# Kernel optimization log

Hardware: AMD Instinct MI355X
Metric: run time of the kernel (lower is better)

The kernel has to match this reference:

```python
import jax, jax.numpy as jnp
import numpy as np

INPUT_SIZE = 128
HIDDEN_SIZE = 128
BATCH = 65536


def _xavier(key, shape):
    fan_out, fan_in = shape
    limit = np.sqrt(6.0 / (fan_in + fan_out)).astype(np.float32)
    return jax.random.uniform(key, shape, jnp.float32, -limit, limit)


def setup_inputs() -> dict:
    key = jax.random.key(0)
    ks = jax.random.split(key, 12)
    inp = {
        "x": jax.random.normal(ks[0], (BATCH, INPUT_SIZE), jnp.float32),
        "h_t": jax.random.normal(ks[1], (BATCH, HIDDEN_SIZE), jnp.float32),
        "c_t": jax.random.normal(ks[2], (BATCH, HIDDEN_SIZE), jnp.float32),
        "W_ii": _xavier(ks[3], (HIDDEN_SIZE, INPUT_SIZE)),
        "W_hi": _xavier(ks[4], (HIDDEN_SIZE, HIDDEN_SIZE)),
        "b_i": jnp.zeros((HIDDEN_SIZE,), jnp.float32),
        "W_if": _xavier(ks[5], (HIDDEN_SIZE, INPUT_SIZE)),
        "W_hf": _xavier(ks[6], (HIDDEN_SIZE, HIDDEN_SIZE)),
        "b_f": jnp.zeros((HIDDEN_SIZE,), jnp.float32),
        "W_ig": _xavier(ks[7], (HIDDEN_SIZE, INPUT_SIZE)),
        "W_hg": _xavier(ks[8], (HIDDEN_SIZE, HIDDEN_SIZE)),
        "b_g": jnp.zeros((HIDDEN_SIZE,), jnp.float32),
        "W_io": _xavier(ks[9], (HIDDEN_SIZE, INPUT_SIZE)),
        "W_ho": _xavier(ks[10], (HIDDEN_SIZE, HIDDEN_SIZE)),
        "b_o": jnp.zeros((HIDDEN_SIZE,), jnp.float32),
    }
    return inp


def reference(x, h_t, c_t, W_ii, W_hi, b_i, W_if, W_hf, b_f, W_ig, W_hg, b_g, W_io, W_ho, b_o):
    # Fuse the 8 small GEMMs into 2 concatenated GEMMs, identical math to
    # per-gate F.linear calls (same weights, just stacked along output dim).
    W_x = jnp.concatenate([W_ii, W_if, W_ig, W_io], axis=0)   # [4H, I]
    W_h = jnp.concatenate([W_hi, W_hf, W_hg, W_ho], axis=0)   # [4H, H]
    b = jnp.concatenate([b_i, b_f, b_g, b_o], axis=0)         # [4H]
    gates = x @ W_x.T + h_t @ W_h.T + b                       # [B, 4H]
    i_a, f_a, g_a, o_a = jnp.split(gates, 4, axis=1)
    i_t = jax.nn.sigmoid(i_a)
    f_t = jax.nn.sigmoid(f_a)
    g_t = jnp.tanh(g_a)
    o_t = jax.nn.sigmoid(o_a)
    c_new = f_t * c_t + i_t * g_t
    h_new = o_t * jnp.tanh(c_new)
    return (h_new, c_new)
```

## Files before the change

### kernel.cpp

```cpp
#include <hip/hip_runtime.h>
#include <hip/hip_bf16.h>


typedef short s16x8 __attribute__((ext_vector_type(8)));
typedef float f32x4 __attribute__((ext_vector_type(4)));

__device__ __forceinline__ short f2bf(float f) {
    __hip_bfloat16 h = __float2bfloat16(f);
    return __builtin_bit_cast(short, h);
}
__device__ __forceinline__ float sigm(float x) { return 1.0f / (1.0f + __expf(-x)); }
__device__ __forceinline__ float tanh_f(float x) { return 1.0f - 2.0f / (1.0f + __expf(2.0f * x)); }

__device__ __forceinline__ void dma16(const float* g, void* lds) {
    __builtin_amdgcn_global_load_lds(
        (const __attribute__((address_space(1))) void*)g,
        (__attribute__((address_space(3))) void*)lds, 16, 0, 0);
}

__global__ __launch_bounds__(256)
void repack_weights(const float* __restrict__ Wii, const float* __restrict__ Whi,
                    const float* __restrict__ Wif, const float* __restrict__ Whf,
                    const float* __restrict__ Wig, const float* __restrict__ Whg,
                    const float* __restrict__ Wio, const float* __restrict__ Who,
                    short* __restrict__ ws)
{
    const int t   = blockIdx.x * 256 + threadIdx.x;
    const int fi  = t >> 6;
    const int l   = t & 63;
    const int ks  = fi & 7;
    const int g   = (fi >> 3) & 3;
    const int jt  = fi >> 5;
    const int j   = jt * 16 + (l & 15);
    const int k   = ks * 32 + (l >> 4) * 8;

    const float* wx = (g == 0) ? Wii : (g == 1) ? Wif : (g == 2) ? Wig : Wio;
    const float* wh = (g == 0) ? Whi : (g == 1) ? Whf : (g == 2) ? Whg : Who;
    const float* src = (k < 128) ? (wx + (size_t)j * 128 + k)
                                 : (wh + (size_t)j * 128 + (k - 128));
    f32x4 a = *(const f32x4*)src;
    f32x4 b = *(const f32x4*)(src + 4);
    s16x8 v;
#pragma unroll
    for (int q = 0; q < 4; ++q) { v[q] = f2bf(a[q]); v[4 + q] = f2bf(b[q]); }
    *(s16x8*)(ws + (size_t)t * 8) = v;
}

__global__ __launch_bounds__(512, 2)
void lstm_cell_kernel(const float* __restrict__ X,
                      const float* __restrict__ H,
                      const float* __restrict__ C,
                      const float* __restrict__ Bi, const float* __restrict__ Bf,
                      const float* __restrict__ Bg, const float* __restrict__ Bo,
                      const short* __restrict__ WS,
                      float* __restrict__ OutH,
                      float* __restrict__ OutC)
{
    __shared__ __align__(16) char sA[65536];

    const int tid = threadIdx.x;
    const int l   = tid & 63;
    const int w   = tid >> 6;
    const int lj  = l & 15;
    const int lq  = l >> 4;
    const int jw  = w * 16 + lj;
    const int tile0 = blockIdx.x * 8;

    s16x8 wreg[4][8];
    {
        const short* wp = WS + (size_t)(w * 4) * 8 * 512 + l * 8;
#pragma unroll
        for (int g = 0; g < 4; ++g)
#pragma unroll
            for (int ks = 0; ks < 8; ++ks)
                wreg[g][ks] = *(const s16x8*)(wp + (size_t)(g * 8 + ks) * 512);
    }
    const float bi  = Bi[jw];
    const float bfv = Bf[jw];
    const float bg  = Bg[jw];
    const float bo  = Bo[jw];

    const int   ci    = l & 31;
    const float* abase = (l >= 32) ? H : X;

    auto STAGE = [&](int t) {
        const int B0 = (tile0 + t) * 32;
        char* dst = sA + (t & 1) * 32768;
#pragma unroll
        for (int r = 0; r < 4; ++r) {
            const int m = w * 4 + r;
            const float* src = abase + (size_t)(B0 + m) * 128 + ((ci ^ (m & 7)) << 2);
            dma16(src, dst + m * 1024);
        }
    };

    float cp[2][8];
    auto CLOAD = [&](int t, float* c) {
        const int B0 = (tile0 + t) * 32;
#pragma unroll
        for (int mt = 0; mt < 2; ++mt)
#pragma unroll
            for (int r = 0; r < 4; ++r)
                c[mt * 4 + r] = C[(size_t)(B0 + mt * 16 + lq * 4 + r) * 128 + jw];
    };

    STAGE(0);  CLOAD(0, cp[0]);
    STAGE(1);  CLOAD(1, cp[1]);

#pragma unroll 2
    for (int t = 0; t < 8; ++t) {
        if (t == 0)      asm volatile("s_waitcnt vmcnt(0)" ::: "memory");
        else if (t == 7) asm volatile("s_waitcnt vmcnt(16)" ::: "memory");
        else             asm volatile("s_waitcnt vmcnt(28)" ::: "memory");
        __builtin_amdgcn_sched_barrier(0);
        __builtin_amdgcn_s_barrier();
        __builtin_amdgcn_sched_barrier(0);

        const char* sb = sA + (t & 1) * 32768;

        f32x4 acc[2][4];
#pragma unroll
        for (int mt = 0; mt < 2; ++mt)
#pragma unroll
            for (int g = 0; g < 4; ++g)
                acc[mt][g] = (f32x4){0.f, 0.f, 0.f, 0.f};

#pragma unroll
        for (int ks = 0; ks < 8; ++ks) {
            s16x8 af[2];
#pragma unroll
            for (int mt = 0; mt < 2; ++mt) {
                const int m  = mt * 16 + lj;
                const int cg = ks * 8 + lq * 2;
                const int p0 = (cg & 32) | ((cg & 31) ^ (m & 7));
                const f32x4 q0 = *(const f32x4*)(sb + m * 1024 + p0 * 16);
                const f32x4 q1 = *(const f32x4*)(sb + m * 1024 + (p0 ^ 1) * 16);
                s16x8 v;
#pragma unroll
                for (int q = 0; q < 4; ++q) { v[q] = f2bf(q0[q]); v[4 + q] = f2bf(q1[q]); }
                af[mt] = v;
            }
#pragma unroll
            for (int g = 0; g < 4; ++g) {
                acc[0][g] = __builtin_amdgcn_mfma_f32_16x16x32_bf16(af[0], wreg[g][ks], acc[0][g], 0, 0, 0);
                acc[1][g] = __builtin_amdgcn_mfma_f32_16x16x32_bf16(af[1], wreg[g][ks], acc[1][g], 0, 0, 0);
            }
        }

        __builtin_amdgcn_sched_barrier(0);
        __builtin_amdgcn_s_barrier();
        __builtin_amdgcn_sched_barrier(0);

        {
            const int B0 = (tile0 + t) * 32;
#pragma unroll
            for (int mt = 0; mt < 2; ++mt) {
#pragma unroll
                for (int r = 0; r < 4; ++r) {
                    const int b = B0 + mt * 16 + lq * 4 + r;
                    const size_t idx = (size_t)b * 128 + jw;
                    const float ia = acc[mt][0][r] + bi;
                    const float fa = acc[mt][1][r] + bfv;
                    const float ga = acc[mt][2][r] + bg;
                    const float oa = acc[mt][3][r] + bo;
                    const float it = sigm(ia);
                    const float ft = sigm(fa);
                    const float gt = tanh_f(ga);
                    const float ot = sigm(oa);
                    const float co = cp[t & 1][mt * 4 + r];
                    const float cn = ft * co + it * gt;
                    const float hn = ot * tanh_f(cn);
                    OutH[idx] = hn;
                    OutC[idx] = cn;
                }
            }
        }

        __builtin_amdgcn_sched_barrier(0);
        if (t < 6) {
            STAGE(t + 2);
            CLOAD(t + 2, cp[t & 1]);
        }
        __builtin_amdgcn_sched_barrier(0);
    }
}

extern "C" void kernel_launch(void* const* d_in, const int* in_sizes, int n_in,
                              void* d_out, int out_size, void* d_ws, size_t ws_size,
                              hipStream_t stream) {
    const float* X   = (const float*)d_in[0];
    const float* H   = (const float*)d_in[1];
    const float* C   = (const float*)d_in[2];
    const float* Wii = (const float*)d_in[3];
    const float* Whi = (const float*)d_in[4];
    const float* Bi  = (const float*)d_in[5];
    const float* Wif = (const float*)d_in[6];
    const float* Whf = (const float*)d_in[7];
    const float* Bf  = (const float*)d_in[8];
    const float* Wig = (const float*)d_in[9];
    const float* Whg = (const float*)d_in[10];
    const float* Bg  = (const float*)d_in[11];
    const float* Wio = (const float*)d_in[12];
    const float* Who = (const float*)d_in[13];
    const float* Bo  = (const float*)d_in[14];

    short* ws = (short*)d_ws;

    hipLaunchKernelGGL(repack_weights, dim3(64), dim3(256), 0, stream,
                       Wii, Whi, Wif, Whf, Wig, Whg, Wio, Who, ws);

    float* OutH = (float*)d_out;
    float* OutC = OutH + (size_t)65536 * 128;

    hipLaunchKernelGGL(lstm_cell_kernel, dim3(256), dim3(512), 0, stream,
                       X, H, C, Bi, Bf, Bg, Bo, ws, OutH, OutC);
}
```

Baseline: 185.0 us.

## Stage activations as bf16 in LDS via registers and halve per-block work

Replaces the direct global-to-LDS DMA of fp32 activations with register loads that are converted to bf16 before being written to LDS in MFMA fragment order, halving the LDS footprint and removing per-k-step conversions and swizzle math. Only half the weight fragments stay resident in registers; the other half are reloaded from global memory each tile to cut register pressure. The launch bound rises to 4 blocks per CU and the grid doubles to 512 blocks of 4 tiles each, aiming for more occupancy to hide latency. In exchange the kernel drops its explicit two-deep DMA prefetch and waitcnt scheduling, and the C load is no longer prefetched a tile ahead.

```diff
diff --git a/kernel.cpp b/kernel.cpp
--- a/kernel.cpp
+++ b/kernel.cpp
@@ -11,12 +11,6 @@
 }
 __device__ __forceinline__ float sigm(float x) { return 1.0f / (1.0f + __expf(-x)); }
 __device__ __forceinline__ float tanh_f(float x) { return 1.0f - 2.0f / (1.0f + __expf(2.0f * x)); }
-
-__device__ __forceinline__ void dma16(const float* g, void* lds) {
-    __builtin_amdgcn_global_load_lds(
-        (const __attribute__((address_space(1))) void*)g,
-        (__attribute__((address_space(3))) void*)lds, 16, 0, 0);
-}
 
 __global__ __launch_bounds__(256)
 void repack_weights(const float* __restrict__ Wii, const float* __restrict__ Whi,
@@ -46,7 +40,7 @@
     *(s16x8*)(ws + (size_t)t * 8) = v;
 }
 
-__global__ __launch_bounds__(512, 2)
+__global__ __launch_bounds__(512, 4)
 void lstm_cell_kernel(const float* __restrict__ X,
                       const float* __restrict__ H,
                       const float* __restrict__ C,
@@ -56,7 +50,7 @@
                       float* __restrict__ OutH,
                       float* __restrict__ OutC)
 {
-    __shared__ __align__(16) char sA[65536];
+    __shared__ __align__(16) char sA[32768];
 
     const int tid = threadIdx.x;
     const int l   = tid & 63;
@@ -64,59 +58,76 @@
     const int lj  = l & 15;
     const int lq  = l >> 4;
     const int jw  = w * 16 + lj;
-    const int tile0 = blockIdx.x * 8;
-
-    s16x8 wreg[4][8];
-    {
-        const short* wp = WS + (size_t)(w * 4) * 8 * 512 + l * 8;
-#pragma unroll
-        for (int g = 0; g < 4; ++g)
-#pragma unroll
-            for (int ks = 0; ks < 8; ++ks)
-                wreg[g][ks] = *(const s16x8*)(wp + (size_t)(g * 8 + ks) * 512);
-    }
+    const int tile0 = blockIdx.x * 4;
+
+    const short* wsw = WS + (size_t)(w * 4) * 8 * 512 + (size_t)l * 8;
+    s16x8 wlo[4][4];
+#pragma unroll
+    for (int g = 0; g < 4; ++g)
+#pragma unroll
+        for (int ks = 0; ks < 4; ++ks)
+            wlo[g][ks] = *(const s16x8*)(wsw + (size_t)(g * 8 + ks) * 512);
+
     const float bi  = Bi[jw];
     const float bfv = Bf[jw];
     const float bg  = Bg[jw];
     const float bo  = Bo[jw];
 
-    const int   ci    = l & 31;
-    const float* abase = (l >= 32) ? H : X;
-
-    auto STAGE = [&](int t) {
+    const float* sbase = (w < 4) ? X : H;
+    const int    colr  = (w & 3) * 32 + lq * 8;
+
+    f32x4 sa[2][2], sb[2][2];
+
+    {
+        const int B0 = tile0 * 32;
+#pragma unroll
+        for (int mt = 0; mt < 2; ++mt) {
+            const float* p = sbase + (size_t)(B0 + mt * 16 + lj) * 128 + colr;
+            sa[0][mt] = *(const f32x4*)p;
+            sb[0][mt] = *(const f32x4*)(p + 4);
+        }
+    }
+
+#pragma unroll
+    for (int t = 0; t < 4; ++t) {
+        char* buf = sA + (t & 1) * 16384;
+
+#pragma unroll
+        for (int mt = 0; mt < 2; ++mt) {
+            s16x8 v;
+#pragma unroll
+            for (int q = 0; q < 4; ++q) {
+                v[q]     = f2bf(sa[t & 1][mt][q]);
+                v[4 + q] = f2bf(sb[t & 1][mt][q]);
+            }
+            *(s16x8*)(buf + (mt * 8 + w) * 1024 + l * 16) = v;
+        }
+        __syncthreads();
+
+        if (t < 3) {
+            const int B0n = (tile0 + t + 1) * 32;
+#pragma unroll
+            for (int mt = 0; mt < 2; ++mt) {
+                const float* p = sbase + (size_t)(B0n + mt * 16 + lj) * 128 + colr;
+                sa[(t + 1) & 1][mt] = *(const f32x4*)p;
+                sb[(t + 1) & 1][mt] = *(const f32x4*)(p + 4);
+            }
+        }
+
+        s16x8 whi[4][4];
+#pragma unroll
+        for (int g = 0; g < 4; ++g)
+#pragma unroll
+            for (int ks = 0; ks < 4; ++ks)
+                whi[g][ks] = *(const s16x8*)(wsw + (size_t)(g * 8 + 4 + ks) * 512);
+
         const int B0 = (tile0 + t) * 32;
-        char* dst = sA + (t & 1) * 32768;
-#pragma unroll
-        for (int r = 0; r < 4; ++r) {
-            const int m = w * 4 + r;
-            const float* src = abase + (size_t)(B0 + m) * 128 + ((ci ^ (m & 7)) << 2);
-            dma16(src, dst + m * 1024);
-        }
-    };
-
-    float cp[2][8];
-    auto CLOAD = [&](int t, float* c) {
-        const int B0 = (tile0 + t) * 32;
+        float cpv[8];
 #pragma unroll
         for (int mt = 0; mt < 2; ++mt)
 #pragma unroll
             for (int r = 0; r < 4; ++r)
-                c[mt * 4 + r] = C[(size_t)(B0 + mt * 16 + lq * 4 + r) * 128 + jw];
-    };
-
-    STAGE(0);  CLOAD(0, cp[0]);
-    STAGE(1);  CLOAD(1, cp[1]);
-
-#pragma unroll 2
-    for (int t = 0; t < 8; ++t) {
-        if (t == 0)      asm volatile("s_waitcnt vmcnt(0)" ::: "memory");
-        else if (t == 7) asm volatile("s_waitcnt vmcnt(16)" ::: "memory");
-        else             asm volatile("s_waitcnt vmcnt(28)" ::: "memory");
-        __builtin_amdgcn_sched_barrier(0);
-        __builtin_amdgcn_s_barrier();
-        __builtin_amdgcn_sched_barrier(0);
-
-        const char* sb = sA + (t & 1) * 32768;
+                cpv[mt * 4 + r] = C[(size_t)(B0 + mt * 16 + lq * 4 + r) * 128 + jw];
 
         f32x4 acc[2][4];
 #pragma unroll
@@ -127,61 +138,37 @@
 
 #pragma unroll
         for (int ks = 0; ks < 8; ++ks) {
-            s16x8 af[2];
-#pragma unroll
-            for (int mt = 0; mt < 2; ++mt) {
-                const int m  = mt * 16 + lj;
-                const int cg = ks * 8 + lq * 2;
-                const int p0 = (cg & 32) | ((cg & 31) ^ (m & 7));
-                const f32x4 q0 = *(const f32x4*)(sb + m * 1024 + p0 * 16);
-                const f32x4 q1 = *(const f32x4*)(sb + m * 1024 + (p0 ^ 1) * 16);
-                s16x8 v;
-#pragma unroll
-                for (int q = 0; q < 4; ++q) { v[q] = f2bf(q0[q]); v[4 + q] = f2bf(q1[q]); }
-                af[mt] = v;
-            }
+            const s16x8 af0 = *(const s16x8*)(buf + (0 * 8 + ks) * 1024 + l * 16);
+            const s16x8 af1 = *(const s16x8*)(buf + (1 * 8 + ks) * 1024 + l * 16);
 #pragma unroll
             for (int g = 0; g < 4; ++g) {
-                acc[0][g] = __builtin_amdgcn_mfma_f32_16x16x32_bf16(af[0], wreg[g][ks], acc[0][g], 0, 0, 0);
-                acc[1][g] = __builtin_amdgcn_mfma_f32_16x16x32_bf16(af[1], wreg[g][ks], acc[1][g], 0, 0, 0);
-            }
-        }
-
-        __builtin_amdgcn_sched_barrier(0);
-        __builtin_amdgcn_s_barrier();
-        __builtin_amdgcn_sched_barrier(0);
-
-        {
-            const int B0 = (tile0 + t) * 32;
-#pragma unroll
-            for (int mt = 0; mt < 2; ++mt) {
-#pragma unroll
-                for (int r = 0; r < 4; ++r) {
-                    const int b = B0 + mt * 16 + lq * 4 + r;
-                    const size_t idx = (size_t)b * 128 + jw;
-                    const float ia = acc[mt][0][r] + bi;
-                    const float fa = acc[mt][1][r] + bfv;
-                    const float ga = acc[mt][2][r] + bg;
-                    const float oa = acc[mt][3][r] + bo;
-                    const float it = sigm(ia);
-                    const float ft = sigm(fa);
-                    const float gt = tanh_f(ga);
-                    const float ot = sigm(oa);
-                    const float co = cp[t & 1][mt * 4 + r];
-                    const float cn = ft * co + it * gt;
-                    const float hn = ot * tanh_f(cn);
-                    OutH[idx] = hn;
-                    OutC[idx] = cn;
-                }
-            }
-        }
-
-        __builtin_amdgcn_sched_barrier(0);
-        if (t < 6) {
-            STAGE(t + 2);
-            CLOAD(t + 2, cp[t & 1]);
-        }
-        __builtin_amdgcn_sched_barrier(0);
+                const s16x8 bfrag = (ks < 4) ? wlo[g][ks] : whi[g][ks - 4];
+                acc[0][g] = __builtin_amdgcn_mfma_f32_16x16x32_bf16(af0, bfrag, acc[0][g], 0, 0, 0);
+                acc[1][g] = __builtin_amdgcn_mfma_f32_16x16x32_bf16(af1, bfrag, acc[1][g], 0, 0, 0);
+            }
+        }
+
+#pragma unroll
+        for (int mt = 0; mt < 2; ++mt) {
+#pragma unroll
+            for (int r = 0; r < 4; ++r) {
+                const int b = B0 + mt * 16 + lq * 4 + r;
+                const size_t idx = (size_t)b * 128 + jw;
+                const float ia = acc[mt][0][r] + bi;
+                const float fa = acc[mt][1][r] + bfv;
+                const float ga = acc[mt][2][r] + bg;
+                const float oa = acc[mt][3][r] + bo;
+                const float it = sigm(ia);
+                const float ft = sigm(fa);
+                const float gt = tanh_f(ga);
+                const float ot = sigm(oa);
+                const float co = cpv[mt * 4 + r];
+                const float cn = ft * co + it * gt;
+                const float hn = ot * tanh_f(cn);
+                OutH[idx] = hn;
+                OutC[idx] = cn;
+            }
+        }
     }
 }
 
@@ -212,6 +199,6 @@
     float* OutH = (float*)d_out;
     float* OutC = OutH + (size_t)65536 * 128;
 
-    hipLaunchKernelGGL(lstm_cell_kernel, dim3(256), dim3(512), 0, stream,
+    hipLaunchKernelGGL(lstm_cell_kernel, dim3(512), dim3(512), 0, stream,
                        X, H, C, Bi, Bf, Bg, Bo, ws, OutH, OutC);
 }
```

After: 232.1 us. +25.5%, slower.
